# Optimization experiments

Hardware: AMD Instinct MI355X
Metric: run time of the kernel (lower is better)

Reference implementation:

```python
import jax, jax.numpy as jnp
import numpy as np

HEADS = 16
THETA = 10000.0


def _rope(x, pos):
    # x: [b, h, s, d_k], pos: [b, s] int
    d_k = x.shape[-1]
    inv_freq = 1.0 / (THETA ** (jnp.arange(0, d_k, 2, dtype=jnp.float32) / d_k))  # [d_k/2]
    ang = pos[..., None].astype(jnp.float32) * inv_freq                           # [b, s, d_k/2]
    cos = jnp.cos(ang)[:, None, :, :]  # [b, 1, s, d_k/2] broadcast over heads
    sin = jnp.sin(ang)[:, None, :, :]
    x_even = x[..., 0::2]
    x_odd = x[..., 1::2]
    r_even = x_even * cos - x_odd * sin
    r_odd = x_even * sin + x_odd * cos
    return jnp.stack([r_even, r_odd], axis=-1).reshape(x.shape)


def setup_inputs() -> dict:
    key = jax.random.key(0)
    ks = jax.random.split(key, 5)
    B, S, D = 4, 2048, 1024
    std = float(np.sqrt(1.0 / D))
    def w(k):
        return jnp.clip(jax.random.normal(k, (D, D), jnp.float32) * std, -3 * std, 3 * std)
    return {
        "x": jax.random.normal(ks[0], (B, S, D), jnp.float32),
        "token_positions": jnp.broadcast_to(jnp.arange(S, dtype=jnp.int32), (B, S)),
        "wq": w(ks[1]),
        "wk": w(ks[2]),
        "wv": w(ks[3]),
        "wo": w(ks[4]),
    }


def reference(x, token_positions, wq, wk, wv, wo):
    B, S, D = x.shape
    h = HEADS
    dk = D // h
    # Projections: einsum 'hd d, ... s d -> ... s hd' == x @ W.T
    def proj(w):
        return jnp.einsum('bsd,kd->bsk', x, w).reshape(B, S, h, dk).transpose(0, 2, 1, 3)
    q = _rope(proj(wq), token_positions)  # [b,h,s,dk]
    k = _rope(proj(wk), token_positions)
    v = proj(wv)
    scores = jnp.einsum('bhqd,bhkd->bhqk', q, k) / np.sqrt(dk).astype(np.float32)
    causal = jnp.tril(jnp.ones((S, S), bool))
    scores = jnp.where(causal, scores, jnp.finfo(scores.dtype).min)
    attn = jax.nn.softmax(scores, axis=-1)
    out = jnp.einsum('bhqk,bhkd->bhqd', attn, v)        # [b,h,s,dk]
    out = out.transpose(0, 2, 1, 3).reshape(B, S, D)    # [b,s,h*dk]
    return jnp.einsum('bsv,dv->bsd', out, wo)
```

## Files before the change

kernel.cpp:

```cpp
#include <hip/hip_runtime.h>
#include <hip/hip_bf16.h>
#include <stdint.h>

typedef __bf16 bf16;
typedef __bf16 bf16x4 __attribute__((ext_vector_type(4)));
typedef __bf16 bf16x8 __attribute__((ext_vector_type(8)));
typedef float f32x4 __attribute__((ext_vector_type(4)));
typedef float f32x16 __attribute__((ext_vector_type(16)));

#define GLDS16(g, l) __builtin_amdgcn_global_load_lds( \
    (const __attribute__((address_space(1))) void*)(g), \
    (__attribute__((address_space(3))) void*)(l), 16, 0, 0)

static constexpr int S = 2048;

__global__ __launch_bounds__(256) void cvt_all(const float* __restrict__ x,
                                               const float* __restrict__ wq,
                                               const float* __restrict__ wk,
                                               const float* __restrict__ wv,
                                               const float* __restrict__ wo,
                                               bf16* __restrict__ xb,
                                               bf16* __restrict__ wqkvb,
                                               bf16* __restrict__ wob) {
  const int bid = blockIdx.x;
  const float* src;
  bf16* dst;
  int i;
  if (bid < 4096) {
    src = x; dst = xb; i = bid * 256 + threadIdx.x;
  } else {
    int w = (bid - 4096) >> 9;
    i = ((bid - 4096) & 511) * 256 + threadIdx.x;
    src = (w == 0) ? wq : (w == 1) ? wk : (w == 2) ? wv : wo;
    dst = (w == 3) ? wob : wqkvb + (size_t)w * 1048576;
  }
  const float4* p = (const float4*)src + (size_t)i * 2;
  float4 a = p[0], b = p[1];
  bf16x8 o;
  o[0] = (bf16)a.x; o[1] = (bf16)a.y; o[2] = (bf16)a.z; o[3] = (bf16)a.w;
  o[4] = (bf16)b.x; o[5] = (bf16)b.y; o[6] = (bf16)b.z; o[7] = (bf16)b.w;
  *((bf16x8*)dst + i) = o;
}

template <int MODE>
__global__ __launch_bounds__(256, 3) void gemm_k(const bf16* __restrict__ xA,
                                                 const bf16* __restrict__ wB,
                                                 const int* __restrict__ tp,
                                                 bf16* __restrict__ oq,
                                                 bf16* __restrict__ ok,
                                                 bf16* __restrict__ ov,
                                                 float* __restrict__ outf) {
  constexpr int K = 1024;
  __shared__ __align__(16) char lds[49152];
  const int t = threadIdx.x, l = t & 63, wid = t >> 6;
  const int wm = wid >> 1, wn = wid & 1;
  const int bm = blockIdx.x, bn = blockIdx.y;

  int sel, tA, tB;
  const bf16 *Ap, *Bp;
  if (MODE == 0) {
    if (bn < 16) {
      sel = bn >> 3;
      tA = bm;
      tB = bn & 7;
      Ap = xA + (size_t)tA * 128 * K;
      Bp = wB + (size_t)(sel * 1024 + tB * 128) * K;
    } else {
      sel = 2;
      tA = bn - 16;
      tB = bm;
      Ap = wB + (size_t)(2048 + tA * 128) * K;
      Bp = xA + (size_t)tB * 128 * K;
    }
  } else {
    sel = 3;
    tA = bm; tB = bn;
    Ap = xA + (size_t)tA * 128 * K;
    Bp = wB + (size_t)tB * 128 * K;
  }

  const int lrow = l >> 2;
  const int csrc = ((l & 3) ^ ((l >> 3) & 3)) * 8;
  const bf16* aS = Ap + (size_t)(wid * 32 + lrow) * K + csrc;
  const bf16* bS = Bp + (size_t)(wid * 32 + lrow) * K + csrc;

  auto stage = [&](int kt, char* base) {
    GLDS16(aS + kt, base + (wid * 32) * 64);
    GLDS16(aS + (size_t)16 * K + kt, base + (wid * 32 + 16) * 64);
    GLDS16(bS + kt, base + 8192 + (wid * 32) * 64);
    GLDS16(bS + (size_t)16 * K + kt, base + 8192 + (wid * 32 + 16) * 64);
  };

  int offA[4], offB[4];
#pragma unroll
  for (int f = 0; f < 4; f++) {
    int ra = wm * 64 + f * 16 + (l & 15);
    offA[f] = ra * 64 + (((l >> 4) ^ ((ra >> 1) & 3)) * 16);
    int rb = wn * 64 + f * 16 + (l & 15);
    offB[f] = 8192 + rb * 64 + (((l >> 4) ^ ((rb >> 1) & 3)) * 16);
  }

  f32x4 acc[4][4] = {};

  char* cur = lds;
  char* nxt = lds + 16384;
  char* ovr = lds + 32768;
  stage(0, cur);
  stage(32, nxt);
#pragma unroll 1
  for (int t_ = 0; t_ < 32; ++t_) {
    if (t_ + 2 < 32) {
      stage((t_ + 2) * 32, ovr);
      asm volatile("s_waitcnt vmcnt(8)" ::: "memory");
    } else if (t_ + 1 < 32) {
      asm volatile("s_waitcnt vmcnt(4)" ::: "memory");
    } else {
      asm volatile("s_waitcnt vmcnt(0)" ::: "memory");
    }
    __builtin_amdgcn_s_barrier();
    __builtin_amdgcn_sched_barrier(0);

    bf16x8 af[4], bg[4];
#pragma unroll
    for (int f = 0; f < 4; f++) {
      af[f] = *(const bf16x8*)(cur + offA[f]);
      bg[f] = *(const bf16x8*)(cur + offB[f]);
    }
    __builtin_amdgcn_s_setprio(1);
#pragma unroll
    for (int mi = 0; mi < 4; mi++)
#pragma unroll
      for (int ni = 0; ni < 4; ni++)
        acc[mi][ni] = __builtin_amdgcn_mfma_f32_16x16x32_bf16(
            af[mi], bg[ni], acc[mi][ni], 0, 0, 0);
    __builtin_amdgcn_s_setprio(0);
    asm volatile("s_waitcnt lgkmcnt(0)" ::: "memory");
    __builtin_amdgcn_sched_barrier(0);
    __builtin_amdgcn_s_barrier();
    char* tmp = cur; cur = nxt; nxt = ovr; ovr = tmp;
  }

  if (MODE == 2) {
    const int rbase = tA * 128 + wm * 64 + (l >> 4) * 4;
    const int cbase = tB * 128 + wn * 64 + (l & 15);
#pragma unroll
    for (int mi = 0; mi < 4; mi++)
#pragma unroll
      for (int ni = 0; ni < 4; ni++)
#pragma unroll
        for (int r = 0; r < 4; r++)
          outf[(size_t)(rbase + mi * 16 + r) * 1024 + cbase + ni * 16] =
              acc[mi][ni][r];
    return;
  }

#pragma unroll
  for (int mi = 0; mi < 4; mi++)
#pragma unroll
    for (int ni = 0; ni < 4; ni++)
#pragma unroll
      for (int r = 0; r < 4; r++) {
        int row = wm * 64 + mi * 16 + (l >> 4) * 4 + r;
        int col = wn * 64 + ni * 16 + (l & 15);
        *(bf16*)(lds + row * 272 + col * 2) = (bf16)acc[mi][ni][r];
      }
  __syncthreads();

#pragma unroll 1
  for (int i = 0; i < 8; ++i) {
    const int id = t + 256 * i;
    const int row = id >> 4, ch = id & 15;
    bf16x8 v8 = *(const bf16x8*)(lds + row * 272 + ch * 16);
    if (sel < 2) {
      const int m = tA * 128 + row;
      const float p = (float)tp[m];
      const int g = ch & 7;
      bf16x8 o;
#pragma unroll
      for (int j = 0; j < 4; j++) {
        float ang = p * exp2f((float)(g * 4 + j) * -0.4152410118609203f);
        float sn, cs;
        sincosf(ang, &sn, &cs);
        float e = (float)v8[2 * j], od = (float)v8[2 * j + 1];
        o[2 * j]     = (bf16)(e * cs - od * sn);
        o[2 * j + 1] = (bf16)(e * sn + od * cs);
      }
      bf16* dst = (sel == 0) ? oq : ok;
      const int h = tB * 2 + (ch >> 3);
      size_t idx = ((size_t)((m >> 11) * 16 + h) << 17) +
                   ((size_t)(m & 2047) << 6) + g * 8;
      *(bf16x8*)(dst + idx) = o;
    } else {
      const int dd = tA * 128 + row;
      const int h = dd >> 6;
      const int s0 = tB * 128 + ch * 8;
      size_t idx = ((size_t)((s0 >> 11) * 16 + h) << 17) +
                   ((size_t)(dd & 63) << 11) + (s0 & 2047);
      *(bf16x8*)(ov + idx) = v8;
    }
  }
}

__global__ __launch_bounds__(512) void attn_k(const bf16* __restrict__ q,
                                              const bf16* __restrict__ k,
                                              const bf16* __restrict__ vt,
                                              bf16* __restrict__ att) {
  __shared__ bf16 Ks[3][4096];
  __shared__ bf16 Vs[3][4096];

  const int t = threadIdx.x, l = t & 63, w = t >> 6;
  const int hi2 = l >> 5, q5 = l & 31;

  const int raw = blockIdx.y * 4 + blockIdx.x;
  const int wg = (raw & 7) * 32 + (raw >> 3);
  const int j_ = wg & 3;
  const int bh = wg >> 2;

  const bf16* qb = q + (size_t)bh * S * 64;
  const bf16* kb = k + (size_t)bh * S * 64;
  const bf16* vb = vt + (size_t)bh * 64 * S;

  const int lrow = l >> 3;
  const int clog = ((l & 7) ^ (lrow & 7)) * 8;

  auto stage = [&](int nt, int b) {
    GLDS16(kb + (size_t)(nt * 64 + w * 8 + lrow) * 64 + clog, &Ks[b][w * 512]);
    GLDS16(vb + (size_t)(w * 8 + lrow) * S + nt * 64 + clog, &Vs[b][w * 512]);
  };

  const int swz = (q5 & 7) << 4;
  int kaddr[4], vaddr[8];
#pragma unroll
  for (int c = 0; c < 4; c++)
    kaddr[c] = q5 * 128 + ((32 * c + 16 * hi2) ^ swz);
#pragma unroll
  for (int m = 0; m < 8; m++)
    vaddr[m] = q5 * 128 + ((16 * m) ^ swz) + 8 * hi2;

  const int b_ = bh >> 4, h_ = bh & 15;
  const char* KsB = (const char*)&Ks[0][0];
  const char* VsB = (const char*)&Vs[0][0];

  for (int pass = 0; pass < 2; ++pass) {
    const int qt = pass ? j_ : 7 - j_;
    const int qrow = qt * 256 + w * 32 + q5;
    bf16x8 qf[4];
#pragma unroll
    for (int c = 0; c < 4; c++) {
      bf16x8 rq = *(const bf16x8*)&qb[(size_t)qrow * 64 + 16 * c + 8 * hi2];
      bf16x8 s_;
#pragma unroll
      for (int j2 = 0; j2 < 8; j2++)
        s_[j2] = (bf16)((float)rq[j2] * 0.18033688011112042f);
      qf[c] = s_;
    }

    f32x16 acc[2] = {};
    float l_r = 0.f;
    const int nkv = 4 * qt + 4;
    const int qmaxw = qt * 256 + w * 32 + 31;

    int cur = 0, nxt = 1, ovr = 2;
    stage(0, 0);
    stage(1, 1);
#pragma unroll 1
    for (int nt = 0; nt < nkv; ++nt) {
      if (nt + 2 < nkv) {
        stage(nt + 2, ovr);
        asm volatile("s_waitcnt vmcnt(4)" ::: "memory");
      } else if (nt + 1 < nkv) {
        asm volatile("s_waitcnt vmcnt(2)" ::: "memory");
      } else {
        asm volatile("s_waitcnt vmcnt(0)" ::: "memory");
      }
      __builtin_amdgcn_s_barrier();
      __builtin_amdgcn_sched_barrier(0);

      const bool live = (64 * nt) <= qmaxw;
      if (live) {
        const int bo = cur * 8192;

        f32x16 sc[2] = {};
        __builtin_amdgcn_s_setprio(1);
#pragma unroll
        for (int c = 0; c < 4; c++) {
#pragma unroll
          for (int T = 0; T < 2; T++) {
            bf16x8 kf = *(const bf16x8*)(KsB + bo + T * 4096 + kaddr[c]);
            sc[T] = __builtin_amdgcn_mfma_f32_32x32x16_bf16(kf, qf[c], sc[T], 0, 0, 0);
          }
        }
        __builtin_amdgcn_s_setprio(0);

        if (64 * nt + 63 > qt * 256 + w * 32) {
#pragma unroll
          for (int T = 0; T < 2; T++)
#pragma unroll
            for (int r = 0; r < 16; r++) {
              int kvg = 64 * nt + 32 * T + (r & 3) + 8 * (r >> 2) + 4 * hi2;
              if (kvg > qrow) sc[T][r] = -1e30f;
            }
        }

        float rs = 0.f;
#pragma unroll
        for (int T = 0; T < 2; T++)
#pragma unroll
          for (int r = 0; r < 16; r++) {
            float pv = __builtin_amdgcn_exp2f(sc[T][r]);
            sc[T][r] = pv;
            rs += pv;
          }
        rs += __shfl_xor(rs, 32);
        l_r += rs;

        bf16x8 pa[4];
#pragma unroll
        for (int c = 0; c < 4; c++)
#pragma unroll
          for (int j2 = 0; j2 < 8; j2++)
            pa[c][j2] = (bf16)sc[c >> 1][8 * (c & 1) + j2];

        __builtin_amdgcn_s_setprio(1);
#pragma unroll
        for (int c = 0; c < 4; c++) {
#pragma unroll
          for (int dt = 0; dt < 2; dt++) {
            bf16x4 v0 = *(const bf16x4*)(VsB + bo + dt * 4096 + vaddr[2 * c]);
            bf16x4 v1 = *(const bf16x4*)(VsB + bo + dt * 4096 + vaddr[2 * c + 1]);
            bf16x8 bv;
#pragma unroll
            for (int j2 = 0; j2 < 4; j2++) { bv[j2] = v0[j2]; bv[4 + j2] = v1[j2]; }
            acc[dt] = __builtin_amdgcn_mfma_f32_32x32x16_bf16(pa[c], bv, acc[dt], 0, 0, 0);
          }
        }
        __builtin_amdgcn_s_setprio(0);
      }

      asm volatile("s_waitcnt lgkmcnt(0)" ::: "memory");
      __builtin_amdgcn_sched_barrier(0);
      __builtin_amdgcn_s_barrier();
      int t3 = cur; cur = nxt; nxt = ovr; ovr = t3;
    }

    float linv = 1.f / l_r;
#pragma unroll
    for (int r = 0; r < 16; r++) {
      int rmap = (r & 3) + 8 * (r >> 2) + 4 * hi2;
      float li = __shfl(linv, rmap);
      int rowq = qt * 256 + w * 32 + rmap;
      size_t rb = ((size_t)(b_ * S + rowq) << 10) + h_ * 64 + q5;
#pragma unroll
      for (int dt = 0; dt < 2; dt++)
        att[rb + 32 * dt] = (bf16)(acc[dt][r] * li);
    }
  }
}

extern "C" void kernel_launch(void* const* d_in, const int* in_sizes, int n_in,
                              void* d_out, int out_size, void* d_ws, size_t ws_size,
                              hipStream_t stream) {
  const float* x  = (const float*)d_in[0];
  const int* tp   = (const int*)d_in[1];
  const float* wq = (const float*)d_in[2];
  const float* wk = (const float*)d_in[3];
  const float* wv = (const float*)d_in[4];
  const float* wo = (const float*)d_in[5];
  float* out = (float*)d_out;

  char* ws = (char*)d_ws;
  const size_t TEN = 16777216;
  bf16* x_bf    = (bf16*)(ws);
  bf16* q_bf    = (bf16*)(ws + TEN);
  bf16* k_bf    = (bf16*)(ws + 2 * TEN);
  bf16* v_bf    = (bf16*)(ws + 3 * TEN);
  bf16* wqkv_bf = (bf16*)(ws + 4 * TEN);
  bf16* wo_bf   = wqkv_bf + 3 * 1048576;
  bf16* att_bf  = x_bf;

  cvt_all<<<6144, 256, 0, stream>>>(x, wq, wk, wv, wo, x_bf, wqkv_bf, wo_bf);

  dim3 gq(64, 24);
  gemm_k<0><<<gq, 256, 0, stream>>>(x_bf, wqkv_bf, tp, q_bf, k_bf, v_bf,
                                    nullptr);

  dim3 ga(4, 64);
  attn_k<<<ga, 512, 0, stream>>>(q_bf, k_bf, v_bf, att_bf);

  dim3 go(64, 8);
  gemm_k<2><<<go, 256, 0, stream>>>(att_bf, wo_bf, nullptr, nullptr, nullptr,
                                    nullptr, out);
}
```

Baseline: 160.0 us.

## Precompute RoPE tables and split attention into one q-tile per block

RoPE cos/sin values are computed once per position into bf16 tables by extra blocks in the conversion kernel, and the QKV GEMM epilogue reads them instead of calling sincosf per element. The attention kernel drops its two-pass loop: each of 512 blocks now handles a single 256-row query tile, with heavy and light tiles ordered across the grid. It also gains a launch-bounds occupancy hint and processes score halves one at a time to lower register pressure. The change adds a small table read and trades per-block load pairing for more, unevenly sized blocks. Rounding the tables to bf16 adds a little error to the rotation.

```diff
diff --git a/kernel.cpp b/kernel.cpp
--- a/kernel.cpp
+++ b/kernel.cpp
@@ -19,10 +19,24 @@
                                                const float* __restrict__ wk,
                                                const float* __restrict__ wv,
                                                const float* __restrict__ wo,
+                                               const int* __restrict__ tp,
                                                bf16* __restrict__ xb,
                                                bf16* __restrict__ wqkvb,
-                                               bf16* __restrict__ wob) {
+                                               bf16* __restrict__ wob,
+                                               bf16* __restrict__ tabc,
+                                               bf16* __restrict__ tabs) {
   const int bid = blockIdx.x;
+  if (bid >= 6144) {
+    int idx = (bid - 6144) * 256 + threadIdx.x;
+    int row = idx >> 5, pp = idx & 31;
+    float p = (float)tp[row];
+    float ang = p * exp2f((float)pp * -0.4152410118609203f);
+    float sn, cs;
+    sincosf(ang, &sn, &cs);
+    tabc[idx] = (bf16)cs;
+    tabs[idx] = (bf16)sn;
+    return;
+  }
   const float* src;
   bf16* dst;
   int i;
@@ -45,7 +59,8 @@
 template <int MODE>
 __global__ __launch_bounds__(256, 3) void gemm_k(const bf16* __restrict__ xA,
                                                  const bf16* __restrict__ wB,
-                                                 const int* __restrict__ tp,
+                                                 const bf16* __restrict__ tabc,
+                                                 const bf16* __restrict__ tabs,
                                                  bf16* __restrict__ oq,
                                                  bf16* __restrict__ ok,
                                                  bf16* __restrict__ ov,
@@ -166,21 +181,20 @@
       }
   __syncthreads();
 
-#pragma unroll 1
+#pragma unroll 2
   for (int i = 0; i < 8; ++i) {
     const int id = t + 256 * i;
     const int row = id >> 4, ch = id & 15;
     bf16x8 v8 = *(const bf16x8*)(lds + row * 272 + ch * 16);
     if (sel < 2) {
       const int m = tA * 128 + row;
-      const float p = (float)tp[m];
       const int g = ch & 7;
+      bf16x4 tc = *(const bf16x4*)(tabc + m * 32 + g * 4);
+      bf16x4 tsn = *(const bf16x4*)(tabs + m * 32 + g * 4);
       bf16x8 o;
 #pragma unroll
       for (int j = 0; j < 4; j++) {
-        float ang = p * exp2f((float)(g * 4 + j) * -0.4152410118609203f);
-        float sn, cs;
-        sincosf(ang, &sn, &cs);
+        float cs = (float)tc[j], sn = (float)tsn[j];
         float e = (float)v8[2 * j], od = (float)v8[2 * j + 1];
         o[2 * j]     = (bf16)(e * cs - od * sn);
         o[2 * j + 1] = (bf16)(e * sn + od * cs);
@@ -201,20 +215,21 @@
   }
 }
 
-__global__ __launch_bounds__(512) void attn_k(const bf16* __restrict__ q,
-                                              const bf16* __restrict__ k,
-                                              const bf16* __restrict__ vt,
-                                              bf16* __restrict__ att) {
+__global__ __launch_bounds__(512, 4) void attn_k(const bf16* __restrict__ q,
+                                                 const bf16* __restrict__ k,
+                                                 const bf16* __restrict__ vt,
+                                                 bf16* __restrict__ att) {
   __shared__ bf16 Ks[3][4096];
   __shared__ bf16 Vs[3][4096];
 
   const int t = threadIdx.x, l = t & 63, w = t >> 6;
   const int hi2 = l >> 5, q5 = l & 31;
 
-  const int raw = blockIdx.y * 4 + blockIdx.x;
-  const int wg = (raw & 7) * 32 + (raw >> 3);
-  const int j_ = wg & 3;
-  const int bh = wg >> 2;
+  const int raw = blockIdx.x;
+  const int r2 = raw & 255;
+  const int wg = (r2 & 7) * 32 + (r2 >> 3);
+  const int bh = ((raw < 256) ? 0 : 32) + (wg >> 3);
+  const int qt = (raw < 256) ? (wg & 7) : 7 - (wg & 7);
 
   const bf16* qb = q + (size_t)bh * S * 64;
   const bf16* kb = k + (size_t)bh * S * 64;
@@ -241,119 +256,110 @@
   const char* KsB = (const char*)&Ks[0][0];
   const char* VsB = (const char*)&Vs[0][0];
 
-  for (int pass = 0; pass < 2; ++pass) {
-    const int qt = pass ? j_ : 7 - j_;
-    const int qrow = qt * 256 + w * 32 + q5;
-    bf16x8 qf[4];
-#pragma unroll
-    for (int c = 0; c < 4; c++) {
-      bf16x8 rq = *(const bf16x8*)&qb[(size_t)qrow * 64 + 16 * c + 8 * hi2];
-      bf16x8 s_;
-#pragma unroll
-      for (int j2 = 0; j2 < 8; j2++)
-        s_[j2] = (bf16)((float)rq[j2] * 0.18033688011112042f);
-      qf[c] = s_;
-    }
-
-    f32x16 acc[2] = {};
-    float l_r = 0.f;
-    const int nkv = 4 * qt + 4;
-    const int qmaxw = qt * 256 + w * 32 + 31;
-
-    int cur = 0, nxt = 1, ovr = 2;
-    stage(0, 0);
-    stage(1, 1);
+  const int wqbase = qt * 256 + w * 32;
+  const int qrow = wqbase + q5;
+  bf16x8 qf[4];
+#pragma unroll
+  for (int c = 0; c < 4; c++) {
+    bf16x8 rq = *(const bf16x8*)&qb[(size_t)qrow * 64 + 16 * c + 8 * hi2];
+    bf16x8 s_;
+#pragma unroll
+    for (int j2 = 0; j2 < 8; j2++)
+      s_[j2] = (bf16)((float)rq[j2] * 0.18033688011112042f);
+    qf[c] = s_;
+  }
+
+  f32x16 acc[2] = {};
+  float l_r = 0.f;
+  const int nkv = 4 * qt + 4;
+  const int qmaxw = wqbase + 31;
+
+  int cur = 0, nxt = 1, ovr = 2;
+  stage(0, 0);
+  stage(1, 1);
 #pragma unroll 1
-    for (int nt = 0; nt < nkv; ++nt) {
-      if (nt + 2 < nkv) {
-        stage(nt + 2, ovr);
-        asm volatile("s_waitcnt vmcnt(4)" ::: "memory");
-      } else if (nt + 1 < nkv) {
-        asm volatile("s_waitcnt vmcnt(2)" ::: "memory");
-      } else {
-        asm volatile("s_waitcnt vmcnt(0)" ::: "memory");
-      }
-      __builtin_amdgcn_s_barrier();
-      __builtin_amdgcn_sched_barrier(0);
-
-      const bool live = (64 * nt) <= qmaxw;
-      if (live) {
-        const int bo = cur * 8192;
-
-        f32x16 sc[2] = {};
+  for (int nt = 0; nt < nkv; ++nt) {
+    if (nt + 2 < nkv) {
+      stage(nt + 2, ovr);
+      asm volatile("s_waitcnt vmcnt(4)" ::: "memory");
+    } else if (nt + 1 < nkv) {
+      asm volatile("s_waitcnt vmcnt(2)" ::: "memory");
+    } else {
+      asm volatile("s_waitcnt vmcnt(0)" ::: "memory");
+    }
+    __builtin_amdgcn_s_barrier();
+    __builtin_amdgcn_sched_barrier(0);
+
+    const bool live = (64 * nt) <= qmaxw;
+    if (live) {
+      const int bo = cur * 8192;
+      float rs = 0.f;
+#pragma unroll
+      for (int T = 0; T < 2; T++) {
+        f32x16 sc = {};
         __builtin_amdgcn_s_setprio(1);
 #pragma unroll
         for (int c = 0; c < 4; c++) {
-#pragma unroll
-          for (int T = 0; T < 2; T++) {
-            bf16x8 kf = *(const bf16x8*)(KsB + bo + T * 4096 + kaddr[c]);
-            sc[T] = __builtin_amdgcn_mfma_f32_32x32x16_bf16(kf, qf[c], sc[T], 0, 0, 0);
+          bf16x8 kf = *(const bf16x8*)(KsB + bo + T * 4096 + kaddr[c]);
+          sc = __builtin_amdgcn_mfma_f32_32x32x16_bf16(kf, qf[c], sc, 0, 0, 0);
+        }
+        __builtin_amdgcn_s_setprio(0);
+
+        if (64 * nt + 32 * T + 31 > wqbase) {
+#pragma unroll
+          for (int r = 0; r < 16; r++) {
+            int kvg = 64 * nt + 32 * T + (r & 3) + 8 * (r >> 2) + 4 * hi2;
+            if (kvg > qrow) sc[r] = -1e30f;
           }
         }
-        __builtin_amdgcn_s_setprio(0);
-
-        if (64 * nt + 63 > qt * 256 + w * 32) {
-#pragma unroll
-          for (int T = 0; T < 2; T++)
-#pragma unroll
-            for (int r = 0; r < 16; r++) {
-              int kvg = 64 * nt + 32 * T + (r & 3) + 8 * (r >> 2) + 4 * hi2;
-              if (kvg > qrow) sc[T][r] = -1e30f;
-            }
+
+        bf16x8 pa0, pa1;
+#pragma unroll
+        for (int r = 0; r < 8; r++) {
+          float p0 = __builtin_amdgcn_exp2f(sc[r]);
+          float p1 = __builtin_amdgcn_exp2f(sc[8 + r]);
+          rs += p0 + p1;
+          pa0[r] = (bf16)p0;
+          pa1[r] = (bf16)p1;
         }
 
-        float rs = 0.f;
-#pragma unroll
-        for (int T = 0; T < 2; T++)
-#pragma unroll
-          for (int r = 0; r < 16; r++) {
-            float pv = __builtin_amdgcn_exp2f(sc[T][r]);
-            sc[T][r] = pv;
-            rs += pv;
-          }
-        rs += __shfl_xor(rs, 32);
-        l_r += rs;
-
-        bf16x8 pa[4];
-#pragma unroll
-        for (int c = 0; c < 4; c++)
-#pragma unroll
-          for (int j2 = 0; j2 < 8; j2++)
-            pa[c][j2] = (bf16)sc[c >> 1][8 * (c & 1) + j2];
-
         __builtin_amdgcn_s_setprio(1);
 #pragma unroll
-        for (int c = 0; c < 4; c++) {
-#pragma unroll
-          for (int dt = 0; dt < 2; dt++) {
-            bf16x4 v0 = *(const bf16x4*)(VsB + bo + dt * 4096 + vaddr[2 * c]);
-            bf16x4 v1 = *(const bf16x4*)(VsB + bo + dt * 4096 + vaddr[2 * c + 1]);
-            bf16x8 bv;
-#pragma unroll
-            for (int j2 = 0; j2 < 4; j2++) { bv[j2] = v0[j2]; bv[4 + j2] = v1[j2]; }
-            acc[dt] = __builtin_amdgcn_mfma_f32_32x32x16_bf16(pa[c], bv, acc[dt], 0, 0, 0);
-          }
+        for (int dt = 0; dt < 2; dt++) {
+          bf16x4 v0 = *(const bf16x4*)(VsB + bo + dt * 4096 + vaddr[4 * T]);
+          bf16x4 v1 = *(const bf16x4*)(VsB + bo + dt * 4096 + vaddr[4 * T + 1]);
+          bf16x8 bv;
+#pragma unroll
+          for (int j2 = 0; j2 < 4; j2++) { bv[j2] = v0[j2]; bv[4 + j2] = v1[j2]; }
+          acc[dt] = __builtin_amdgcn_mfma_f32_32x32x16_bf16(pa0, bv, acc[dt], 0, 0, 0);
+          v0 = *(const bf16x4*)(VsB + bo + dt * 4096 + vaddr[4 * T + 2]);
+          v1 = *(const bf16x4*)(VsB + bo + dt * 4096 + vaddr[4 * T + 3]);
+#pragma unroll
+          for (int j2 = 0; j2 < 4; j2++) { bv[j2] = v0[j2]; bv[4 + j2] = v1[j2]; }
+          acc[dt] = __builtin_amdgcn_mfma_f32_32x32x16_bf16(pa1, bv, acc[dt], 0, 0, 0);
         }
         __builtin_amdgcn_s_setprio(0);
       }
-
-      asm volatile("s_waitcnt lgkmcnt(0)" ::: "memory");
-      __builtin_amdgcn_sched_barrier(0);
-      __builtin_amdgcn_s_barrier();
-      int t3 = cur; cur = nxt; nxt = ovr; ovr = t3;
-    }
-
-    float linv = 1.f / l_r;
-#pragma unroll
-    for (int r = 0; r < 16; r++) {
-      int rmap = (r & 3) + 8 * (r >> 2) + 4 * hi2;
-      float li = __shfl(linv, rmap);
-      int rowq = qt * 256 + w * 32 + rmap;
-      size_t rb = ((size_t)(b_ * S + rowq) << 10) + h_ * 64 + q5;
-#pragma unroll
-      for (int dt = 0; dt < 2; dt++)
-        att[rb + 32 * dt] = (bf16)(acc[dt][r] * li);
-    }
+      rs += __shfl_xor(rs, 32);
+      l_r += rs;
+    }
+
+    asm volatile("s_waitcnt lgkmcnt(0)" ::: "memory");
+    __builtin_amdgcn_sched_barrier(0);
+    __builtin_amdgcn_s_barrier();
+    int t3 = cur; cur = nxt; nxt = ovr; ovr = t3;
+  }
+
+  float linv = 1.f / l_r;
+#pragma unroll
+  for (int r = 0; r < 16; r++) {
+    int rmap = (r & 3) + 8 * (r >> 2) + 4 * hi2;
+    float li = __shfl(linv, rmap);
+    int rowq = wqbase + rmap;
+    size_t rb = ((size_t)(b_ * S + rowq) << 10) + h_ * 64 + q5;
+#pragma unroll
+    for (int dt = 0; dt < 2; dt++)
+      att[rb + 32 * dt] = (bf16)(acc[dt][r] * li);
   }
 }
 
@@ -376,18 +382,20 @@
   bf16* v_bf    = (bf16*)(ws + 3 * TEN);
   bf16* wqkv_bf = (bf16*)(ws + 4 * TEN);
   bf16* wo_bf   = wqkv_bf + 3 * 1048576;
+  bf16* tabc    = wo_bf + 1048576;
+  bf16* tabs    = tabc + 262144;
   bf16* att_bf  = x_bf;
 
-  cvt_all<<<6144, 256, 0, stream>>>(x, wq, wk, wv, wo, x_bf, wqkv_bf, wo_bf);
+  cvt_all<<<7168, 256, 0, stream>>>(x, wq, wk, wv, wo, tp, x_bf, wqkv_bf,
+                                    wo_bf, tabc, tabs);
 
   dim3 gq(64, 24);
-  gemm_k<0><<<gq, 256, 0, stream>>>(x_bf, wqkv_bf, tp, q_bf, k_bf, v_bf,
-                                    nullptr);
-
-  dim3 ga(4, 64);
-  attn_k<<<ga, 512, 0, stream>>>(q_bf, k_bf, v_bf, att_bf);
+  gemm_k<0><<<gq, 256, 0, stream>>>(x_bf, wqkv_bf, tabc, tabs, q_bf, k_bf,
+                                    v_bf, nullptr);
+
+  attn_k<<<512, 512, 0, stream>>>(q_bf, k_bf, v_bf, att_bf);
 
   dim3 go(64, 8);
   gemm_k<2><<<go, 256, 0, stream>>>(att_bf, wo_bf, nullptr, nullptr, nullptr,
-                                    nullptr, out);
+                                    nullptr, nullptr, out);
 }
```

New measurement: 154.4 us. -3.5%, faster.
